# Kernel tuning notes

Measured on AMD Instinct MI355X. Metric: run time of the kernel, lower is better.

## Reference

```python
import jax, jax.numpy as jnp
import numpy as np
import math

NUM_ROTATIONS = 8
STRIDE = 1
PADDING = 1


def _rotate_weights(weight, num_rotations):
    """Bilinear rotation of conv filters, matching torch affine_grid/grid_sample
    with align_corners=False and zero padding.

    weight: (O, I, k, k) -> returns (R, O, I, k, k)
    """
    O, I, k, _ = weight.shape
    dt = weight.dtype
    # align_corners=False normalized pixel-center coords in [-1, 1]
    c = (2.0 * jnp.arange(k, dtype=jnp.float32) + 1.0) / k - 1.0
    ygrid, xgrid = jnp.meshgrid(c, c, indexing='ij')          # (k, k)
    angles = 2.0 * math.pi * jnp.arange(num_rotations, dtype=jnp.float32) / num_rotations
    cos = jnp.cos(angles)[:, None, None]                       # (R,1,1)
    sin = jnp.sin(angles)[:, None, None]
    # theta = [[cos, -sin, 0], [sin, cos, 0]] applied to (x, y, 1)
    xs = cos * xgrid - sin * ygrid                             # (R,k,k)
    ys = sin * xgrid + cos * ygrid
    # unnormalize (align_corners=False): ix = ((x+1)*W - 1)/2
    ix = ((xs + 1.0) * k - 1.0) * 0.5
    iy = ((ys + 1.0) * k - 1.0) * 0.5
    ix0f = jnp.floor(ix); iy0f = jnp.floor(iy)
    wx1 = (ix - ix0f).astype(dt); wy1 = (iy - iy0f).astype(dt)
    wx0 = 1.0 - wx1; wy0 = 1.0 - wy1
    ix0 = ix0f.astype(jnp.int32); iy0 = iy0f.astype(jnp.int32)
    ix1 = ix0 + 1; iy1 = iy0 + 1

    def gather(iyc, ixc):
        valid = ((iyc >= 0) & (iyc < k) & (ixc >= 0) & (ixc < k)).astype(dt)
        iycl = jnp.clip(iyc, 0, k - 1)
        ixcl = jnp.clip(ixc, 0, k - 1)
        # advanced indexing broadcasts: (O, I, R, k, k)
        return weight[:, :, iycl, ixcl] * valid

    out = (gather(iy0, ix0) * (wy0 * wx0)
           + gather(iy0, ix1) * (wy0 * wx1)
           + gather(iy1, ix0) * (wy1 * wx0)
           + gather(iy1, ix1) * (wy1 * wx1))                   # (O,I,R,k,k)
    return jnp.transpose(out, (2, 0, 1, 3, 4))                 # (R,O,I,k,k)


def setup_inputs() -> dict:
    key = jax.random.key(0)
    k1, k2 = jax.random.split(key)
    x = jax.random.normal(k1, (4, 256, 128, 128), dtype=jnp.float32)
    weight = jax.random.normal(k2, (256, 256, 3, 3), dtype=jnp.float32)
    return {"x": x, "weight": weight}


def reference(x, weight):
    R = NUM_ROTATIONS
    O, I, k, _ = weight.shape
    rw = _rotate_weights(weight, R)                            # (R,O,I,k,k)
    rw_flat = rw.reshape(R * O, I, k, k)
    # one conv for all rotations (same input), then max over rotations
    out = jax.lax.conv_general_dilated(
        x, rw_flat,
        window_strides=(STRIDE, STRIDE),
        padding=[(PADDING, PADDING), (PADDING, PADDING)],
        dimension_numbers=('NCHW', 'OIHW', 'NCHW'))           # (B, R*O, H', W')
    B, _, Hp, Wp = out.shape
    out = out.reshape(B, R, O, Hp, Wp)
    return jnp.max(out, axis=1)                                # (B, O, H', W')
```

## Files before the change

kernel.cpp:

```cpp
#include <hip/hip_runtime.h>
#include <hip/hip_bf16.h>
#include <math.h>

typedef __attribute__((ext_vector_type(8))) short bf16x8;
typedef __attribute__((ext_vector_type(4))) float f32x4;

#define R_TOTAL 8
#define CIN     256
#define COUT    256
#define HH      128
#define WW      128
#define BB      4
#define MTOT    (COUT * R_TOTAL)
#define KTAPS   9

#define XSZ   (3 * 130 * 32)
#define ABUF  (128 * 32)

__device__ __forceinline__ void g2l16(void* lds, const void* g) {
    __builtin_amdgcn_global_load_lds(
        (const __attribute__((address_space(1))) unsigned int*)g,
        (__attribute__((address_space(3))) unsigned int*)lds,
        16, 0, 0);
}

__global__ __launch_bounds__(256)
void to_nhwc_bf16(const float* __restrict__ x, __hip_bfloat16* __restrict__ xb) {
    __shared__ __hip_bfloat16 t[32][33];
    const int b  = blockIdx.z;
    const int c0 = blockIdx.y * 32;
    const int p0 = blockIdx.x * 32;
    const int tx = threadIdx.x & 31;
    const int ty = threadIdx.x >> 5;
    const float* xp = x + (size_t)b * CIN * (HH * WW);
    #pragma unroll
    for (int j = 0; j < 4; ++j) {
        int c = ty * 4 + j;
        t[c][tx] = __float2bfloat16(xp[(size_t)(c0 + c) * (HH * WW) + p0 + tx]);
    }
    __syncthreads();
    __hip_bfloat16* op = xb + ((size_t)b * (HH * WW) + p0) * CIN + c0;
    #pragma unroll
    for (int j = 0; j < 4; ++j) {
        int p = ty * 4 + j;
        op[(size_t)p * CIN + tx] = t[tx][p];
    }
}

__global__ __launch_bounds__(256)
void zero_guard_row(__hip_bfloat16* __restrict__ xb) {
    size_t base = (size_t)BB * HH * WW * CIN;
    int i = blockIdx.x * 256 + threadIdx.x;
    xb[base + i] = __float2bfloat16(0.0f);
}

__global__ __launch_bounds__(256)
void rotate_weights_bf16(const float* __restrict__ w, __hip_bfloat16* __restrict__ rwb) {
    const int i = threadIdx.x;
    const int m = blockIdx.x;
    const int o = m >> 3, r = m & 7;

    float ang = 6.283185307179586f * (float)r / 8.0f;
    float cs = cosf(ang), sn = sinf(ang);

    const float* wp = w + ((size_t)o * CIN + i) * 9;
    __hip_bfloat16* op = rwb + (size_t)m * (KTAPS * CIN) + i;

    #pragma unroll
    for (int ky = 0; ky < 3; ++ky) {
        #pragma unroll
        for (int kx = 0; kx < 3; ++kx) {
            float yg = (2.0f * (float)ky + 1.0f) / 3.0f - 1.0f;
            float xg = (2.0f * (float)kx + 1.0f) / 3.0f - 1.0f;
            float xsf = cs * xg - sn * yg;
            float ysf = sn * xg + cs * yg;
            float ix = ((xsf + 1.0f) * 3.0f - 1.0f) * 0.5f;
            float iy = ((ysf + 1.0f) * 3.0f - 1.0f) * 0.5f;
            float ix0f = floorf(ix), iy0f = floorf(iy);
            float wx1 = ix - ix0f,  wy1 = iy - iy0f;
            float wx0 = 1.0f - wx1, wy0 = 1.0f - wy1;
            int ix0 = (int)ix0f, iy0 = (int)iy0f;
            int ix1 = ix0 + 1,   iy1 = iy0 + 1;
            float acc = 0.0f;
            if (iy0 >= 0 && iy0 < 3 && ix0 >= 0 && ix0 < 3) acc += wp[iy0*3+ix0] * (wy0*wx0);
            if (iy0 >= 0 && iy0 < 3 && ix1 >= 0 && ix1 < 3) acc += wp[iy0*3+ix1] * (wy0*wx1);
            if (iy1 >= 0 && iy1 < 3 && ix0 >= 0 && ix0 < 3) acc += wp[iy1*3+ix0] * (wy1*wx0);
            if (iy1 >= 0 && iy1 < 3 && ix1 >= 0 && ix1 < 3) acc += wp[iy1*3+ix1] * (wy1*wx1);
            op[(ky * 3 + kx) * CIN] = __float2bfloat16(acc);
        }
    }
}

__global__ __launch_bounds__(256)
void rotconv_mfma_kernel(const __hip_bfloat16* __restrict__ xb,
                         const __hip_bfloat16* __restrict__ rwb,
                         float* __restrict__ out) {
    const int tid  = threadIdx.x;
    const int lane = tid & 63;
    const int w    = tid >> 6;
    const int wm   = w >> 1;
    const int wn   = w & 1;
    const int q    = lane >> 4, lr = lane & 15;

    const int bid = (blockIdx.x & 7) * 1024 + (blockIdx.x >> 3);
    const int mt  = bid >> 9;
    const int nt  = bid & 511;
    const int b   = nt >> 7;
    const int y0  = nt & 127;
    const int m0  = mt << 7;

    __shared__ __align__(16) __hip_bfloat16 xs[2 * XSZ];
    __shared__ __align__(16) __hip_bfloat16 As[3 * ABUF];

    for (int j = tid; j < 384; j += 256) {
        int bufi = j / 192;
        int rem  = j % 192;
        int row = rem / 64; int colsel = (rem >> 5) & 1; int ch = rem & 31;
        int colL = colsel ? 129 : 0;
        xs[bufi * XSZ + (row * 130 + colL) * 32 + ch] = __float2bfloat16(0.0f);
    }

    int aOff[4];
    #pragma unroll
    for (int mi = 0; mi < 4; ++mi) {
        int row = wm * 64 + mi * 16 + lr;
        aOff[mi] = row * 32 + 8 * (q ^ ((row >> 1) & 3));
    }
    int bOff[4][3];
    #pragma unroll
    for (int ni = 0; ni < 4; ++ni)
        #pragma unroll
        for (int kx = 0; kx < 3; ++kx) {
            int colL = wn * 64 + ni * 16 + lr + kx;
            bOff[ni][kx] = colL * 32 + 8 * (q ^ ((colL >> 1) & 3));
        }

    const int arow0 = w * 32 + (lane >> 2);
    const int arow1 = w * 32 + 16 + (lane >> 2);
    const int dstA0 = (w * 32) * 32;
    const int dstA1 = (w * 32 + 16) * 32;
    const __hip_bfloat16* srcA0 =
        rwb + (size_t)(m0 + arow0) * (KTAPS * CIN) + 8 * ((lane & 3) ^ ((arow0 >> 1) & 3));
    const __hip_bfloat16* srcA1 =
        rwb + (size_t)(m0 + arow1) * (KTAPS * CIN) + 8 * ((lane & 3) ^ ((arow1 >> 1) & 3));

    const __hip_bfloat16* srcX[6];
    int dstX[6];
    #pragma unroll
    for (int j = 0; j < 6; ++j) {
        int id  = j * 4 + w;
        int row = id >> 3;
        int cg  = (id & 7) * 16;
        int gy  = y0 - 1 + row;
        size_t rowIdx = ((unsigned)gy < (unsigned)HH) ? (size_t)(b * HH + gy)
                                                      : (size_t)(BB * HH);
        int gx = cg + (lane >> 2);
        int colL = gx + 1;
        dstX[j] = (row * 130 + 1 + cg) * 32;
        srcX[j] = xb + (rowIdx * WW + gx) * CIN + 8 * ((lane & 3) ^ ((colL >> 1) & 3));
    }

    f32x4 acc[4][4];
    #pragma unroll
    for (int mi = 0; mi < 4; ++mi)
        #pragma unroll
        for (int ni = 0; ni < 4; ++ni) {
            f32x4 z = {0.f, 0.f, 0.f, 0.f};
            acc[mi][ni] = z;
        }

    __syncthreads();

    #pragma unroll
    for (int j = 0; j < 6; ++j) g2l16(xs + dstX[j], srcX[j]);
    g2l16(As + 0 * ABUF + dstA0, srcA0 + 0 * CIN);
    g2l16(As + 0 * ABUF + dstA1, srcA1 + 0 * CIN);
    g2l16(As + 1 * ABUF + dstA0, srcA0 + 1 * CIN);
    g2l16(As + 1 * ABUF + dstA1, srcA1 + 1 * CIN);
    asm volatile("s_waitcnt vmcnt(0)" ::: "memory");
    __syncthreads();

    bf16x8 af0[4], bv0[4], af1[4], bv1[4];
    {
        const __hip_bfloat16* ar = As;
        const __hip_bfloat16* br = xs;
        #pragma unroll
        for (int mi = 0; mi < 4; ++mi) af0[mi] = *(const bf16x8*)(ar + aOff[mi]);
        #pragma unroll
        for (int ni = 0; ni < 4; ++ni) bv0[ni] = *(const bf16x8*)(br + bOff[ni][0]);
    }

#define TAP(P, NW, DOA, DOX, DORD, XW, XR, CAf, CBv, RAf, RBv)                 \
  {                                                                            \
    if (DOA) {                                                                 \
      const int aofs = (((P) + 2) < 9) ? (((P) + 2) * CIN + c * 32)            \
                                       : ((((P) + 2) - 9) * CIN + (c + 1) * 32);\
      __hip_bfloat16* ab = As + (((P) + 2) % 3) * ABUF;                        \
      g2l16(ab + dstA0, srcA0 + aofs);                                         \
      g2l16(ab + dstA1, srcA1 + aofs);                                         \
    }                                                                          \
    if (DOX) g2l16(xs + (XW) * XSZ + dstX[(P) > 0 ? (P) - 1 : 0],              \
                   srcX[(P) > 0 ? (P) - 1 : 0] + (c + 1) * 32);                \
    asm volatile("s_waitcnt vmcnt(%0)" :: "i"(NW) : "memory");                 \
    asm volatile("s_barrier" ::: "memory");                                    \
    if (DORD) {                                                                \
      const __hip_bfloat16* ar = As + ((((P) + 1) % 3)) * ABUF;                \
      const __hip_bfloat16* br = xs + (XR) * XSZ                               \
                                 + (((((P) + 1) % 9)) / 3) * (130 * 32);       \
      _Pragma("unroll")                                                        \
      for (int mi = 0; mi < 4; ++mi) RAf[mi] = *(const bf16x8*)(ar + aOff[mi]);\
      _Pragma("unroll")                                                        \
      for (int ni = 0; ni < 4; ++ni)                                           \
          RBv[ni] = *(const bf16x8*)(br + bOff[ni][(((P) + 1) % 9) % 3]);      \
    }                                                                          \
    __builtin_amdgcn_s_setprio(1);                                             \
    _Pragma("unroll")                                                          \
    for (int mi = 0; mi < 4; ++mi)                                             \
      _Pragma("unroll")                                                        \
      for (int ni = 0; ni < 4; ++ni)                                           \
        acc[mi][ni] = __builtin_amdgcn_mfma_f32_16x16x32_bf16(                 \
            CAf[mi], CBv[ni], acc[mi][ni], 0, 0, 0);                           \
    __builtin_amdgcn_s_setprio(0);                                             \
  }

#define CHK0                                                                   \
    TAP(0, 2, 1, 0, 1, 1, 0, af0, bv0, af1, bv1)                               \
    TAP(1, 3, 1, 1, 1, 1, 0, af1, bv1, af0, bv0)                               \
    TAP(2, 3, 1, 1, 1, 1, 0, af0, bv0, af1, bv1)                               \
    TAP(3, 3, 1, 1, 1, 1, 0, af1, bv1, af0, bv0)                               \
    TAP(4, 3, 1, 1, 1, 1, 0, af0, bv0, af1, bv1)                               \
    TAP(5, 3, 1, 1, 1, 1, 0, af1, bv1, af0, bv0)                               \
    TAP(6, 3, 1, 1, 1, 1, 0, af0, bv0, af1, bv1)                               \
    TAP(7, 2, 1, 0, 1, 1, 0, af1, bv1, af0, bv0)                               \
    TAP(8, 2, 1, 0, 1, 1, 1, af0, bv0, af1, bv1)

#define CHK1                                                                   \
    TAP(0, 2, 1, 0, 1, 0, 1, af1, bv1, af0, bv0)                               \
    TAP(1, 3, 1, 1, 1, 0, 1, af0, bv0, af1, bv1)                               \
    TAP(2, 3, 1, 1, 1, 0, 1, af1, bv1, af0, bv0)                               \
    TAP(3, 3, 1, 1, 1, 0, 1, af0, bv0, af1, bv1)                               \
    TAP(4, 3, 1, 1, 1, 0, 1, af1, bv1, af0, bv0)                               \
    TAP(5, 3, 1, 1, 1, 0, 1, af0, bv0, af1, bv1)                               \
    TAP(6, 3, 1, 1, 1, 0, 1, af1, bv1, af0, bv0)                               \
    TAP(7, 2, 1, 0, 1, 0, 1, af0, bv0, af1, bv1)                               \
    TAP(8, 2, 1, 0, 1, 0, 0, af1, bv1, af0, bv0)

#define CHKT                                                                   \
    TAP(0, 2, 1, 0, 1, 0, 1, af1, bv1, af0, bv0)                               \
    TAP(1, 2, 1, 0, 1, 0, 1, af0, bv0, af1, bv1)                               \
    TAP(2, 2, 1, 0, 1, 0, 1, af1, bv1, af0, bv0)                               \
    TAP(3, 2, 1, 0, 1, 0, 1, af0, bv0, af1, bv1)                               \
    TAP(4, 2, 1, 0, 1, 0, 1, af1, bv1, af0, bv0)                               \
    TAP(5, 2, 1, 0, 1, 0, 1, af0, bv0, af1, bv1)                               \
    TAP(6, 2, 1, 0, 1, 0, 1, af1, bv1, af0, bv0)                               \
    TAP(7, 0, 0, 0, 1, 0, 1, af0, bv0, af1, bv1)                               \
    {                                                                          \
      __builtin_amdgcn_s_setprio(1);                                           \
      _Pragma("unroll")                                                        \
      for (int mi = 0; mi < 4; ++mi)                                           \
        _Pragma("unroll")                                                      \
        for (int ni = 0; ni < 4; ++ni)                                         \
          acc[mi][ni] = __builtin_amdgcn_mfma_f32_16x16x32_bf16(               \
              af1[mi], bv1[ni], acc[mi][ni], 0, 0, 0);                         \
      __builtin_amdgcn_s_setprio(0);                                           \
    }

    { const int c = 0; CHK0 }
    { const int c = 1; CHK1 }
    { const int c = 2; CHK0 }
    { const int c = 3; CHK1 }
    { const int c = 4; CHK0 }
    { const int c = 5; CHK1 }
    { const int c = 6; CHK0 }
    { const int c = 7; CHKT }

#undef TAP
#undef CHK0
#undef CHK1
#undef CHKT

    const int oBase = (m0 + wm * 64) >> 3;
    #pragma unroll
    for (int mi = 0; mi < 4; ++mi) {
        #pragma unroll
        for (int ni = 0; ni < 4; ++ni) {
            f32x4 a4 = acc[mi][ni];
            float v = fmaxf(fmaxf(a4[0], a4[1]), fmaxf(a4[2], a4[3]));
            v = fmaxf(v, __shfl_xor(v, 16));
            if ((q & 1) == 0) {
                int o = oBase + mi * 2 + (q >> 1);
                int colc = wn * 64 + ni * 16 + lr;
                out[(((size_t)(b * COUT + o)) * HH + y0) * WW + colc] = v;
            }
        }
    }
}

__global__ void rotate_weights_kernel(const float* __restrict__ w,
                                      float* __restrict__ rw,
                                      int r0, int rcount) {
    int idx = blockIdx.x * blockDim.x + threadIdx.x;
    int total = COUT * CIN * rcount;
    if (idx >= total) return;
    int rr = idx % rcount;
    int ii = (idx / rcount) % CIN;
    int oo = idx / (rcount * CIN);
    int r  = r0 + rr;
    float ang = 6.283185307179586f * (float)r / 8.0f;
    float cs = cosf(ang), sn = sinf(ang);
    const float* wp = w  + ((size_t)oo * CIN + ii) * 9;
    float*       op = rw + (((size_t)oo * CIN + ii) * rcount + rr) * 9;
    #pragma unroll
    for (int ky = 0; ky < 3; ++ky)
        #pragma unroll
        for (int kx = 0; kx < 3; ++kx) {
            float yg = (2.0f * ky + 1.0f) / 3.0f - 1.0f;
            float xg = (2.0f * kx + 1.0f) / 3.0f - 1.0f;
            float xsf = cs * xg - sn * yg;
            float ysf = sn * xg + cs * yg;
            float ix = ((xsf + 1.0f) * 3.0f - 1.0f) * 0.5f;
            float iy = ((ysf + 1.0f) * 3.0f - 1.0f) * 0.5f;
            float ix0f = floorf(ix), iy0f = floorf(iy);
            float wx1 = ix - ix0f,  wy1 = iy - iy0f;
            float wx0 = 1.0f - wx1, wy0 = 1.0f - wy1;
            int ix0 = (int)ix0f, iy0 = (int)iy0f;
            int ix1 = ix0 + 1,   iy1 = iy0 + 1;
            float acc = 0.0f;
            if (iy0 >= 0 && iy0 < 3 && ix0 >= 0 && ix0 < 3) acc += wp[iy0*3+ix0]*(wy0*wx0);
            if (iy0 >= 0 && iy0 < 3 && ix1 >= 0 && ix1 < 3) acc += wp[iy0*3+ix1]*(wy0*wx1);
            if (iy1 >= 0 && iy1 < 3 && ix0 >= 0 && ix0 < 3) acc += wp[iy1*3+ix0]*(wy1*wx0);
            if (iy1 >= 0 && iy1 < 3 && ix1 >= 0 && ix1 < 3) acc += wp[iy1*3+ix1]*(wy1*wx1);
            op[ky * 3 + kx] = acc;
        }
}

template <int RCOUNT>
__global__ __launch_bounds__(256)
void rotconv_max_kernel(const float* __restrict__ x,
                        const float* __restrict__ rw,
                        float* __restrict__ out,
                        int first) {
    const int tid = threadIdx.x;
    const int tx = tid & 15;
    const int ty = tid >> 4;
    const int x0 = blockIdx.x * 32;
    const int y0 = blockIdx.y * 32;
    const int o  = blockIdx.z % COUT;
    const int b  = blockIdx.z / COUT;
    __shared__ float xsm[34][36];
    float acc[RCOUNT][2][2];
    #pragma unroll
    for (int r = 0; r < RCOUNT; ++r)
        #pragma unroll
        for (int py = 0; py < 2; ++py)
            #pragma unroll
            for (int px = 0; px < 2; ++px) acc[r][py][px] = 0.0f;
    for (int i = 0; i < CIN; ++i) {
        __syncthreads();
        const float* xp = x + ((size_t)(b * CIN + i)) * (HH * WW);
        for (int idx = tid; idx < 34 * 34; idx += 256) {
            int row = idx / 34, col = idx - row * 34;
            int gy = y0 - 1 + row, gx = x0 - 1 + col;
            float v = 0.0f;
            if (gy >= 0 && gy < HH && gx >= 0 && gx < WW) v = xp[gy * WW + gx];
            xsm[row][col] = v;
        }
        __syncthreads();
        float xv[4][4];
        #pragma unroll
        for (int ry = 0; ry < 4; ++ry)
            #pragma unroll
            for (int cx = 0; cx < 4; ++cx) xv[ry][cx] = xsm[ty*2+ry][tx*2+cx];
        const float* wp = rw + ((size_t)(o * CIN + i)) * (RCOUNT * 9);
        #pragma unroll
        for (int r = 0; r < RCOUNT; ++r) {
            float wv[9];
            #pragma unroll
            for (int t2 = 0; t2 < 9; ++t2) wv[t2] = wp[r * 9 + t2];
            #pragma unroll
            for (int py = 0; py < 2; ++py)
                #pragma unroll
                for (int px = 0; px < 2; ++px) {
                    float a = acc[r][py][px];
                    #pragma unroll
                    for (int ky = 0; ky < 3; ++ky)
                        #pragma unroll
                        for (int kx = 0; kx < 3; ++kx)
                            a += xv[py+ky][px+kx] * wv[ky*3+kx];
                    acc[r][py][px] = a;
                }
        }
    }
    #pragma unroll
    for (int py = 0; py < 2; ++py)
        #pragma unroll
        for (int px = 0; px < 2; ++px) {
            float m = acc[0][py][px];
            #pragma unroll
            for (int r = 1; r < RCOUNT; ++r) m = fmaxf(m, acc[r][py][px]);
            int oy = y0 + ty * 2 + py;
            int ox = x0 + tx * 2 + px;
            float* op = out + (((size_t)(b * COUT + o)) * HH + oy) * WW + ox;
            if (first) *op = m;
            else       *op = fmaxf(*op, m);
        }
}

extern "C" void kernel_launch(void* const* d_in, const int* in_sizes, int n_in,
                              void* d_out, int out_size, void* d_ws, size_t ws_size,
                              hipStream_t stream) {
    const float* x = (const float*)d_in[0];
    const float* w = (const float*)d_in[1];
    float* out = (float*)d_out;

    const size_t xbBytes = ((size_t)BB * HH * WW + WW) * CIN * sizeof(__hip_bfloat16);
    const size_t rwBytes = (size_t)MTOT * KTAPS * CIN * sizeof(__hip_bfloat16);

    if (ws_size >= xbBytes + rwBytes) {
        __hip_bfloat16* xbuf = (__hip_bfloat16*)d_ws;
        __hip_bfloat16* rwb  = (__hip_bfloat16*)((char*)d_ws + xbBytes);

        to_nhwc_bf16<<<dim3((HH * WW) / 32, CIN / 32, BB), 256, 0, stream>>>(x, xbuf);
        zero_guard_row<<<(WW * CIN) / 256, 256, 0, stream>>>(w ? xbuf : xbuf);
        rotate_weights_bf16<<<MTOT, 256, 0, stream>>>(w, rwb);
        rotconv_mfma_kernel<<<8192, 256, 0, stream>>>(xbuf, rwb, out);
        return;
    }

    float* rw = (float*)d_ws;
    int chunk = 8;
    while (chunk > 1 && (size_t)COUT * CIN * chunk * 9 * sizeof(float) > ws_size)
        chunk >>= 1;
    int first = 1;
    for (int r0 = 0; r0 < R_TOTAL; r0 += chunk) {
        int rc = chunk;
        int total = COUT * CIN * rc;
        rotate_weights_kernel<<<(total + 255) / 256, 256, 0, stream>>>(w, rw, r0, rc);
        dim3 grid(WW / 32, HH / 32, BB * COUT);
        switch (rc) {
            case 8: rotconv_max_kernel<8><<<grid, 256, 0, stream>>>(x, rw, out, first); break;
            case 4: rotconv_max_kernel<4><<<grid, 256, 0, stream>>>(x, rw, out, first); break;
            case 2: rotconv_max_kernel<2><<<grid, 256, 0, stream>>>(x, rw, out, first); break;
            default: rotconv_max_kernel<1><<<grid, 256, 0, stream>>>(x, rw, out, first); break;
        }
        first = 0;
    }
}
```

Measured before the change: 606.4 us.

## Move barrier before prefetch issue and deepen weight prefetch to three stages

Reorders each tap so the wait and barrier come before the next global-to-LDS loads are issued. Weight tiles are now prefetched three taps ahead, filling all three A buffers in the prologue, and the X slab loads are rescheduled to taps 0-5. The aim is one barrier per tap that also protects buffer reuse, with more load latency hidden behind the MFMA work. The risk is subtle hazards in the vmcnt counts and the buffer indices.

```diff
diff --git a/kernel.cpp b/kernel.cpp
--- a/kernel.cpp
+++ b/kernel.cpp
@@ -177,6 +177,8 @@
     g2l16(As + 0 * ABUF + dstA1, srcA1 + 0 * CIN);
     g2l16(As + 1 * ABUF + dstA0, srcA0 + 1 * CIN);
     g2l16(As + 1 * ABUF + dstA1, srcA1 + 1 * CIN);
+    g2l16(As + 2 * ABUF + dstA0, srcA0 + 2 * CIN);
+    g2l16(As + 2 * ABUF + dstA1, srcA1 + 2 * CIN);
     asm volatile("s_waitcnt vmcnt(0)" ::: "memory");
     __syncthreads();
 
@@ -190,23 +192,22 @@
         for (int ni = 0; ni < 4; ++ni) bv0[ni] = *(const bf16x8*)(br + bOff[ni][0]);
     }
 
-#define TAP(P, NW, DOA, DOX, DORD, XW, XR, CAf, CBv, RAf, RBv)                 \
+#define TAP(P, NW, DOA, DOX, XBW, XBR, DORD, CAf, CBv, RAf, RBv)               \
   {                                                                            \
+    asm volatile("s_waitcnt vmcnt(%0)" :: "i"(NW) : "memory");                 \
+    asm volatile("s_barrier" ::: "memory");                                    \
     if (DOA) {                                                                 \
-      const int aofs = (((P) + 2) < 9) ? (((P) + 2) * CIN + c * 32)            \
-                                       : ((((P) + 2) - 9) * CIN + (c + 1) * 32);\
-      __hip_bfloat16* ab = As + (((P) + 2) % 3) * ABUF;                        \
+      __hip_bfloat16* ab = As + ((P) % 3) * ABUF;                              \
+      const int aofs = (((P) + 3) % 9) * CIN + (c + ((P) + 3) / 9) * 32;       \
       g2l16(ab + dstA0, srcA0 + aofs);                                         \
       g2l16(ab + dstA1, srcA1 + aofs);                                         \
     }                                                                          \
-    if (DOX) g2l16(xs + (XW) * XSZ + dstX[(P) > 0 ? (P) - 1 : 0],              \
-                   srcX[(P) > 0 ? (P) - 1 : 0] + (c + 1) * 32);                \
-    asm volatile("s_waitcnt vmcnt(%0)" :: "i"(NW) : "memory");                 \
-    asm volatile("s_barrier" ::: "memory");                                    \
+    if (DOX) g2l16(xs + (XBW) * XSZ + dstX[(P) < 6 ? (P) : 0],                 \
+                   srcX[(P) < 6 ? (P) : 0] + (c + 1) * 32);                    \
     if (DORD) {                                                                \
-      const __hip_bfloat16* ar = As + ((((P) + 1) % 3)) * ABUF;                \
-      const __hip_bfloat16* br = xs + (XR) * XSZ                               \
-                                 + (((((P) + 1) % 9)) / 3) * (130 * 32);       \
+      const __hip_bfloat16* ar = As + (((P) + 1) % 3) * ABUF;                  \
+      const __hip_bfloat16* br = xs + (XBR) * XSZ                              \
+                                 + ((((P) + 1) % 9) / 3) * (130 * 32);         \
       _Pragma("unroll")                                                        \
       for (int mi = 0; mi < 4; ++mi) RAf[mi] = *(const bf16x8*)(ar + aOff[mi]);\
       _Pragma("unroll")                                                        \
@@ -223,55 +224,46 @@
     __builtin_amdgcn_s_setprio(0);                                             \
   }
 
-#define CHK0                                                                   \
-    TAP(0, 2, 1, 0, 1, 1, 0, af0, bv0, af1, bv1)                               \
-    TAP(1, 3, 1, 1, 1, 1, 0, af1, bv1, af0, bv0)                               \
-    TAP(2, 3, 1, 1, 1, 1, 0, af0, bv0, af1, bv1)                               \
-    TAP(3, 3, 1, 1, 1, 1, 0, af1, bv1, af0, bv0)                               \
-    TAP(4, 3, 1, 1, 1, 1, 0, af0, bv0, af1, bv1)                               \
-    TAP(5, 3, 1, 1, 1, 1, 0, af1, bv1, af0, bv0)                               \
-    TAP(6, 3, 1, 1, 1, 1, 0, af0, bv0, af1, bv1)                               \
-    TAP(7, 2, 1, 0, 1, 1, 0, af1, bv1, af0, bv0)                               \
-    TAP(8, 2, 1, 0, 1, 1, 1, af0, bv0, af1, bv1)
+#define CHK0(NW0)                                                              \
+    TAP(0, NW0, 1, 1, 1, 0, 1, af0, bv0, af1, bv1)                             \
+    TAP(1, 3,   1, 1, 1, 0, 1, af1, bv1, af0, bv0)                             \
+    TAP(2, 3,   1, 1, 1, 0, 1, af0, bv0, af1, bv1)                             \
+    TAP(3, 3,   1, 1, 1, 0, 1, af1, bv1, af0, bv0)                             \
+    TAP(4, 3,   1, 1, 1, 0, 1, af0, bv0, af1, bv1)                             \
+    TAP(5, 3,   1, 1, 1, 0, 1, af1, bv1, af0, bv0)                             \
+    TAP(6, 3,   1, 0, 1, 0, 1, af0, bv0, af1, bv1)                             \
+    TAP(7, 2,   1, 0, 1, 0, 1, af1, bv1, af0, bv0)                             \
+    TAP(8, 2,   1, 0, 1, 1, 1, af0, bv0, af1, bv1)
 
 #define CHK1                                                                   \
-    TAP(0, 2, 1, 0, 1, 0, 1, af1, bv1, af0, bv0)                               \
-    TAP(1, 3, 1, 1, 1, 0, 1, af0, bv0, af1, bv1)                               \
-    TAP(2, 3, 1, 1, 1, 0, 1, af1, bv1, af0, bv0)                               \
-    TAP(3, 3, 1, 1, 1, 0, 1, af0, bv0, af1, bv1)                               \
-    TAP(4, 3, 1, 1, 1, 0, 1, af1, bv1, af0, bv0)                               \
-    TAP(5, 3, 1, 1, 1, 0, 1, af0, bv0, af1, bv1)                               \
-    TAP(6, 3, 1, 1, 1, 0, 1, af1, bv1, af0, bv0)                               \
-    TAP(7, 2, 1, 0, 1, 0, 1, af0, bv0, af1, bv1)                               \
-    TAP(8, 2, 1, 0, 1, 0, 0, af1, bv1, af0, bv0)
+    TAP(0, 2, 1, 1, 0, 1, 1, af1, bv1, af0, bv0)                               \
+    TAP(1, 3, 1, 1, 0, 1, 1, af0, bv0, af1, bv1)                               \
+    TAP(2, 3, 1, 1, 0, 1, 1, af1, bv1, af0, bv0)                               \
+    TAP(3, 3, 1, 1, 0, 1, 1, af0, bv0, af1, bv1)                               \
+    TAP(4, 3, 1, 1, 0, 1, 1, af1, bv1, af0, bv0)                               \
+    TAP(5, 3, 1, 1, 0, 1, 1, af0, bv0, af1, bv1)                               \
+    TAP(6, 3, 1, 0, 0, 1, 1, af1, bv1, af0, bv0)                               \
+    TAP(7, 2, 1, 0, 0, 1, 1, af0, bv0, af1, bv1)                               \
+    TAP(8, 2, 1, 0, 0, 0, 1, af1, bv1, af0, bv0)
 
 #define CHKT                                                                   \
-    TAP(0, 2, 1, 0, 1, 0, 1, af1, bv1, af0, bv0)                               \
-    TAP(1, 2, 1, 0, 1, 0, 1, af0, bv0, af1, bv1)                               \
-    TAP(2, 2, 1, 0, 1, 0, 1, af1, bv1, af0, bv0)                               \
-    TAP(3, 2, 1, 0, 1, 0, 1, af0, bv0, af1, bv1)                               \
-    TAP(4, 2, 1, 0, 1, 0, 1, af1, bv1, af0, bv0)                               \
-    TAP(5, 2, 1, 0, 1, 0, 1, af0, bv0, af1, bv1)                               \
-    TAP(6, 2, 1, 0, 1, 0, 1, af1, bv1, af0, bv0)                               \
-    TAP(7, 0, 0, 0, 1, 0, 1, af0, bv0, af1, bv1)                               \
-    {                                                                          \
-      __builtin_amdgcn_s_setprio(1);                                           \
-      _Pragma("unroll")                                                        \
-      for (int mi = 0; mi < 4; ++mi)                                           \
-        _Pragma("unroll")                                                      \
-        for (int ni = 0; ni < 4; ++ni)                                         \
-          acc[mi][ni] = __builtin_amdgcn_mfma_f32_16x16x32_bf16(               \
-              af1[mi], bv1[ni], acc[mi][ni], 0, 0, 0);                         \
-      __builtin_amdgcn_s_setprio(0);                                           \
-    }
-
-    { const int c = 0; CHK0 }
+    TAP(0, 2, 1, 0, 0, 1, 1, af1, bv1, af0, bv0)                               \
+    TAP(1, 2, 1, 0, 0, 1, 1, af0, bv0, af1, bv1)                               \
+    TAP(2, 2, 1, 0, 0, 1, 1, af1, bv1, af0, bv0)                               \
+    TAP(3, 2, 1, 0, 0, 1, 1, af0, bv0, af1, bv1)                               \
+    TAP(4, 2, 1, 0, 0, 1, 1, af1, bv1, af0, bv0)                               \
+    TAP(5, 2, 1, 0, 0, 1, 1, af0, bv0, af1, bv1)                               \
+    TAP(6, 2, 0, 0, 0, 1, 1, af1, bv1, af0, bv0)                               \
+    TAP(7, 0, 0, 0, 0, 1, 1, af0, bv0, af1, bv1)                               \
+    TAP(8, 0, 0, 0, 0, 1, 0, af1, bv1, af0, bv0)
+
+    { const int c = 0; CHK0(0) }
     { const int c = 1; CHK1 }
-    { const int c = 2; CHK0 }
+    { const int c = 2; CHK0(2) }
     { const int c = 3; CHK1 }
-    { const int c = 4; CHK0 }
+    { const int c = 4; CHK0(2) }
     { const int c = 5; CHK1 }
-    { const int c = 6; CHK0 }
+    { const int c = 6; CHK0(2) }
     { const int c = 7; CHKT }
 
 #undef TAP
@@ -421,7 +413,7 @@
         __hip_bfloat16* rwb  = (__hip_bfloat16*)((char*)d_ws + xbBytes);
 
         to_nhwc_bf16<<<dim3((HH * WW) / 32, CIN / 32, BB), 256, 0, stream>>>(x, xbuf);
-        zero_guard_row<<<(WW * CIN) / 256, 256, 0, stream>>>(w ? xbuf : xbuf);
+        zero_guard_row<<<(WW * CIN) / 256, 256, 0, stream>>>(xbuf);
         rotate_weights_bf16<<<MTOT, 256, 0, stream>>>(w, rwb);
         rotconv_mfma_kernel<<<8192, 256, 0, stream>>>(xbuf, rwb, out);
         return;
```

Measured after the change: 658.5 us. 8.6% more time.
